# Kernel optimization log

Measured on AMD Instinct MI355X. Metric: run time of the kernel, lower is better.

Reference implementation:

```python
import jax, jax.numpy as jnp
import numpy as np

IN_C = 64
OUT_C = 64
NUM_RELS = 32
N_NODES = 20000
N_EDGES = 50000


def setup_inputs() -> dict:
    key = jax.random.key(0)
    k1, k2, k3, k4, k5, k6, k7 = jax.random.split(key, 7)
    x = jax.random.normal(k1, (N_NODES, IN_C), dtype=jnp.float32)
    edge_index = jax.random.randint(k2, (2, N_EDGES), 0, N_NODES, dtype=jnp.int64)
    edge_type = jax.random.randint(k3, (N_EDGES,), 0, NUM_RELS, dtype=jnp.int64)
    weight_fwd = jax.random.normal(k4, (NUM_RELS, IN_C * OUT_C), dtype=jnp.float32)
    weight_bwd = jax.random.normal(k5, (NUM_RELS, IN_C * OUT_C), dtype=jnp.float32)
    lin_w = jax.random.normal(k6, (OUT_C, IN_C), dtype=jnp.float32) * (1.0 / np.sqrt(IN_C))
    lin_b = jax.random.normal(k7, (OUT_C,), dtype=jnp.float32) * 0.01
    return {"x": x, "edge_index": edge_index, "edge_type": edge_type,
            "weight_fwd": weight_fwd, "weight_bwd": weight_bwd,
            "lin_w": lin_w, "lin_b": lin_b}


def type_gcn_conv(x, src, dst, edge_type, weight_table):
    # degrees[e] = (# edges sharing src[e]) + 1  (faithful to pairwise-compare count)
    n_nodes = x.shape[0]
    counts = jax.ops.segment_sum(jnp.ones(src.shape[0], jnp.float32), src,
                                 num_segments=n_nodes)
    degrees = counts[src] + 1.0                      # [E]
    w = weight_table[edge_type]                      # [E, in*out] gather
    w = w / (jnp.linalg.norm(w, axis=1, keepdims=True) + 0.01)
    w = w / degrees[:, None]
    w = w.reshape(-1, IN_C, OUT_C)                   # [E, in, out]
    msg = jnp.einsum('ei,eio->eo', x[src], w)        # per-edge small matmul
    return jax.ops.segment_sum(msg, dst, num_segments=n_nodes)  # scatter-add at dst


def reference(x, edge_index, edge_type, weight_fwd, weight_bwd, lin_w, lin_b):
    src, dst = edge_index[0], edge_index[1]
    fwd = type_gcn_conv(x, src, dst, edge_type, weight_fwd)
    # backward conv sees reversed edge_index: its src is original dst
    bwd = type_gcn_conv(x, dst, src, edge_type, weight_bwd)
    return x @ lin_w.T + lin_b + fwd + bwd
```

## Files before the change

### kernel.cpp

```cpp
#include <hip/hip_runtime.h>

#define NREL 32

typedef short short8 __attribute__((ext_vector_type(8)));
typedef float f32x4 __attribute__((ext_vector_type(4)));

__device__ inline unsigned short f2bf(float f) {
    union { float f; unsigned u; } u; u.f = f;
    unsigned r = u.u + 0x7FFF + ((u.u >> 16) & 1);
    return (unsigned short)(r >> 16);
}

__device__ inline void bucket_scan(const int* __restrict__ hist, int lane,
                                   int& h, int& P, int& excl) {
    h = (lane < NREL) ? hist[lane] : 0;
    P = ((h + 63) >> 6) << 6;
    int s = P;
    #pragma unroll
    for (int off = 1; off < 32; off <<= 1) {
        int t = __shfl_up(s, off, 64);
        if ((lane & 31) >= off) s += t;
    }
    excl = s - P;
}


__global__ __launch_bounds__(256) void setup_kernel(
        const float* __restrict__ x,
        const int* __restrict__ src, const int* __restrict__ dst,
        const int* __restrict__ et,
        const float* __restrict__ wf, const float* __restrict__ wb,
        const float* __restrict__ lw, const float* __restrict__ lb,
        float* __restrict__ cntf, float* __restrict__ cntb,
        int* __restrict__ hist, unsigned short* __restrict__ wtb,
        unsigned short* __restrict__ xbf,
        float* __restrict__ out, int E, int N, int nCountB) {
    __shared__ float smem[4 * 8 * 64 + 8];
    int tid = threadIdx.x;
    int b = blockIdx.x;

    if (b < nCountB) {
        int* lh = (int*)smem;
        if (tid < NREL) lh[tid] = 0;
        __syncthreads();
        int e = b * 256 + tid;
        if (e < E) {
            atomicAdd(&cntf[src[e]], 1.0f);
            atomicAdd(&cntb[dst[e]], 1.0f);
            atomicAdd(&lh[et[e]], 1);
        }
        __syncthreads();
        if (tid < NREL && lh[tid]) atomicAdd(&hist[tid], lh[tid]);
        return;
    }
    b -= nCountB;
    if (b < 64) {
        int rel = b & 31, tab = b >> 5;
        const float* s_ = (tab ? wb : wf) + rel * 4096;
        unsigned short* d_ = wtb + (size_t)b * 4096;
        float* part = smem;
        float ssum = 0.f;
        #pragma unroll
        for (int k = 0; k < 16; k += 4) {
            float4 v = *(const float4*)(s_ + tid * 16 + k);
            ssum += v.x * v.x + v.y * v.y + v.z * v.z + v.w * v.w;
        }
        #pragma unroll
        for (int off = 32; off >= 1; off >>= 1) ssum += __shfl_down(ssum, off, 64);
        if ((tid & 63) == 0) part[tid >> 6] = ssum;
        __syncthreads();
        if (tid == 0) part[4] = 1.0f / (sqrtf(part[0] + part[1] + part[2] + part[3]) + 0.01f);
        __syncthreads();
        float sc = part[4];
        int i = tid >> 2, o0 = (tid & 3) * 16;
        #pragma unroll
        for (int q = 0; q < 4; ++q) {
            float4 v = *(const float4*)(s_ + i * 64 + o0 + q * 4);
            d_[(o0 + q * 4 + 0) * 64 + i] = f2bf(v.x * sc);
            d_[(o0 + q * 4 + 1) * 64 + i] = f2bf(v.y * sc);
            d_[(o0 + q * 4 + 2) * 64 + i] = f2bf(v.z * sc);
            d_[(o0 + q * 4 + 3) * 64 + i] = f2bf(v.w * sc);
        }
        return;
    }
    b -= 64;
    {
        int lane = tid & 63, w = tid >> 6;
        int nodeBase = b * 32 + w * 8;
        float4 wrow[16];
        const float4* lwrow = (const float4*)(lw + lane * 64);
        #pragma unroll
        for (int g = 0; g < 16; ++g) wrow[g] = lwrow[g];
        float bias = lb[lane];
        float* xs = smem + w * 8 * 64;
        #pragma unroll
        for (int t = 0; t < 8; ++t) {
            int n = nodeBase + t;
            if (n < N) {
                float v = x[(size_t)n * 64 + lane];
                xs[t * 64 + lane] = v;
                xbf[(size_t)n * 64 + lane] = f2bf(v);
            }
        }
        __syncthreads();
        for (int t = 0; t < 8; ++t) {
            int n = nodeBase + t;
            if (n >= N) break;
            float acc = bias;
            const float4* xr = (const float4*)(xs + t * 64);
            #pragma unroll
            for (int g = 0; g < 16; ++g) {
                float4 xv = xr[g];
                acc = fmaf(xv.x, wrow[g].x, acc);
                acc = fmaf(xv.y, wrow[g].y, acc);
                acc = fmaf(xv.z, wrow[g].z, acc);
                acc = fmaf(xv.w, wrow[g].w, acc);
            }
            out[(size_t)n * 64 + lane] = acc;
        }
    }
}

__global__ void scatter_kernel(const int* __restrict__ src, const int* __restrict__ dst,
                               const int* __restrict__ et,
                               const float* __restrict__ cntf, const float* __restrict__ cntb,
                               int* __restrict__ fill, const int* __restrict__ hist,
                               int4* __restrict__ einfo, int E) {
    __shared__ int lh[NREL];
    __shared__ int lbase[NREL];
    __shared__ int bstartS[NREL];
    int tid = threadIdx.x;
    if (tid < 64) {
        int h, P, excl;
        bucket_scan(hist, tid, h, P, excl);
        if (tid < NREL) bstartS[tid] = excl;
    }
    if (tid < NREL) lh[tid] = 0;
    __syncthreads();
    int e = blockIdx.x * blockDim.x + tid;
    int r = 0, my = 0;
    bool valid = (e < E);
    if (valid) { r = et[e]; my = atomicAdd(&lh[r], 1); }
    __syncthreads();
    if (tid < NREL && lh[tid]) lbase[tid] = atomicAdd(&fill[tid], lh[tid]);
    __syncthreads();
    if (valid) {
        int s = src[e], d = dst[e];
        float invf = 1.0f / (cntf[s] + 1.0f);
        float invb = 1.0f / (cntb[d] + 1.0f);
        einfo[bstartS[r] + lbase[r] + my] =
            make_int4(s, d, __float_as_int(invf), __float_as_int(invb));
    }
}

#define APITCH 72
__global__ __launch_bounds__(256) void conv_mfma(
        const unsigned short* __restrict__ xbf,
        const int* __restrict__ hist,
        const unsigned short* __restrict__ wtb,
        const int4* __restrict__ einfo,
        float* __restrict__ out) {
    int tid = threadIdx.x;
    int lane = tid & 63;
    int h, P, excl;
    bucket_scan(hist, lane, h, P, excl);
    int pos = blockIdx.x * 64;
    unsigned long long m_ = __ballot(lane < NREL && pos >= excl && pos < excl + P);
    if (m_ == 0) return;
    int rel = __ffsll(m_) - 1;
    int start = __shfl(excl, rel, 64);
    int hr = __shfl(h, rel, 64);
    int valid = hr - (pos - start);
    if (valid > 64) valid = 64;
    int dir = blockIdx.y;

    __shared__ unsigned short As[64 * APITCH];
    __shared__ unsigned short Bs[64 * APITCH];
    __shared__ int dstS[64];
    __shared__ float invS[64];

    int j = tid >> 2, part = tid & 3;

    {
        const uint4* s4 = (const uint4*)(wtb + (size_t)((dir << 5) + rel) * 4096 + j * 64 + part * 16);
        uint4 v0 = s4[0], v1 = s4[1];
        *(uint4*)(&Bs[j * APITCH + part * 16]) = v0;
        *(uint4*)(&Bs[j * APITCH + part * 16 + 8]) = v1;
    }

    if (j >= valid) {
        uint4 z = {0, 0, 0, 0};
        *(uint4*)(&As[j * APITCH + part * 16]) = z;
        *(uint4*)(&As[j * APITCH + part * 16 + 8]) = z;
        if (part == 0) { dstS[j] = -1; invS[j] = 0.f; }
    } else {
        int4 v = einfo[pos + j];
        int s_ = dir ? v.y : v.x;
        int d_ = dir ? v.x : v.y;
        float inv = __int_as_float(dir ? v.w : v.z);
        const uint4* xr = (const uint4*)(xbf + (size_t)s_ * 64);
        uint4 a0 = xr[part * 2], a1 = xr[part * 2 + 1];
        *(uint4*)(&As[j * APITCH + part * 16]) = a0;
        *(uint4*)(&As[j * APITCH + part * 16 + 8]) = a1;
        if (part == 0) { dstS[j] = d_; invS[j] = inv; }
    }
    __syncthreads();

    int w = tid >> 6;
    int m = lane & 15, quad = lane >> 4;
    f32x4 acc0 = {0.f, 0.f, 0.f, 0.f}, acc1 = acc0, acc2 = acc0, acc3 = acc0;
    #pragma unroll
    for (int k0 = 0; k0 < 64; k0 += 32) {
        short8 a  = *(const short8*)(&As[(w * 16 + m) * APITCH + k0 + quad * 8]);
        short8 b0 = *(const short8*)(&Bs[(0  + m) * APITCH + k0 + quad * 8]);
        short8 b1 = *(const short8*)(&Bs[(16 + m) * APITCH + k0 + quad * 8]);
        short8 b2 = *(const short8*)(&Bs[(32 + m) * APITCH + k0 + quad * 8]);
        short8 b3 = *(const short8*)(&Bs[(48 + m) * APITCH + k0 + quad * 8]);
        acc0 = __builtin_amdgcn_mfma_f32_16x16x32_bf16(a, b0, acc0, 0, 0, 0);
        acc1 = __builtin_amdgcn_mfma_f32_16x16x32_bf16(a, b1, acc1, 0, 0, 0);
        acc2 = __builtin_amdgcn_mfma_f32_16x16x32_bf16(a, b2, acc2, 0, 0, 0);
        acc3 = __builtin_amdgcn_mfma_f32_16x16x32_bf16(a, b3, acc3, 0, 0, 0);
    }

    int row_base = w * 16 + quad * 4;
    #pragma unroll
    for (int r = 0; r < 4; ++r) {
        int row = row_base + r;
        int d_ = dstS[row];
        if (d_ >= 0) {
            float inv = invS[row];
            float* op = out + (size_t)d_ * 64 + m;
            atomicAdd(op +  0, acc0[r] * inv);
            atomicAdd(op + 16, acc1[r] * inv);
            atomicAdd(op + 32, acc2[r] * inv);
            atomicAdd(op + 48, acc3[r] * inv);
        }
    }
}

extern "C" void kernel_launch(void* const* d_in, const int* in_sizes, int n_in,
                              void* d_out, int out_size, void* d_ws, size_t ws_size,
                              hipStream_t stream) {
    const float* x  = (const float*)d_in[0];
    const int*   ei = (const int*)  d_in[1];
    const int*   et = (const int*)  d_in[2];
    const float* wf = (const float*)d_in[3];
    const float* wb = (const float*)d_in[4];
    const float* lw = (const float*)d_in[5];
    const float* lb = (const float*)d_in[6];
    float* out = (float*)d_out;

    const int E = in_sizes[2];
    const int N = in_sizes[0] / 64;
    const int maxC = ((E + 63) >> 6) + NREL;

    char* p = (char*)d_ws;
    unsigned short* wtb = (unsigned short*)p;  p += (size_t)2 * NREL * 4096 * sizeof(unsigned short);
    unsigned short* xbf = (unsigned short*)p;  p += (size_t)N * 64 * sizeof(unsigned short);
    float* cntf = (float*)p;                   p += (size_t)N * sizeof(float);
    float* cntb = (float*)p;                   p += (size_t)N * sizeof(float);
    int*   hist = (int*)p;                     p += NREL * sizeof(int);
    int*   fill = (int*)p;                     p += NREL * sizeof(int);
    int4*  einfo = (int4*)p;                   p += (size_t)maxC * 64 * sizeof(int4);

    const int* srcp = ei;
    const int* dstp = ei + E;

    hipMemsetAsync(cntf, 0, ((size_t)2 * N + 2 * NREL) * sizeof(float), stream);

    const int nCountB = (E + 255) / 256;
    const int nLinB   = (N + 31) / 32;
    setup_kernel<<<nCountB + 64 + nLinB, 256, 0, stream>>>(
        x, srcp, dstp, et, wf, wb, lw, lb, cntf, cntb, hist, wtb, xbf, out, E, N, nCountB);
    scatter_kernel<<<(E + 255) / 256, 256, 0, stream>>>(
        srcp, dstp, et, cntf, cntb, fill, hist, einfo, E);
    dim3 cgrid(maxC, 2);
    conv_mfma<<<cgrid, 256, 0, stream>>>(xbf, hist, wtb, einfo, out);
}
```

Before: 115.0 us.

## Fuse setup, scatter and conv into one persistent kernel with grid barriers

Replaces the memset and the three kernel launches with a single persistent kernel of 768 blocks. Software grid barriers built on global atomics separate the zeroing, counting/weight-prep/linear, bucket-scatter and MFMA conv phases, which removes launch gaps between them. The conv phase now loads A and B operands straight from global memory into MFMA registers instead of staging them through LDS. The design assumes all 768 blocks are co-resident (launch bounds of 3 blocks per CU). If they are not, the barriers deadlock, and the spin-waits add synchronisation overhead.

```diff
diff --git a/kernel.cpp b/kernel.cpp
--- a/kernel.cpp
+++ b/kernel.cpp
@@ -24,216 +24,216 @@
     excl = s - P;
 }
 
-
-__global__ __launch_bounds__(256) void setup_kernel(
+__device__ inline void grid_barrier(int* bar, int target) {
+    __syncthreads();
+    if (threadIdx.x == 0) {
+        __hip_atomic_fetch_add(bar, 1, __ATOMIC_RELEASE, __HIP_MEMORY_SCOPE_AGENT);
+        while (__hip_atomic_load(bar, __ATOMIC_ACQUIRE, __HIP_MEMORY_SCOPE_AGENT) < target)
+            __builtin_amdgcn_s_sleep(2);
+    }
+    __syncthreads();
+}
+
+
+__global__ __launch_bounds__(256, 3) void fused_kernel(
         const float* __restrict__ x,
         const int* __restrict__ src, const int* __restrict__ dst,
         const int* __restrict__ et,
         const float* __restrict__ wf, const float* __restrict__ wb,
         const float* __restrict__ lw, const float* __restrict__ lb,
-        float* __restrict__ cntf, float* __restrict__ cntb,
-        int* __restrict__ hist, unsigned short* __restrict__ wtb,
-        unsigned short* __restrict__ xbf,
-        float* __restrict__ out, int E, int N, int nCountB) {
+        unsigned short* wtb, unsigned short* xbf,
+        float* cntf, float* cntb, int* hist, int* fill,
+        int* bar, int4* einfo, float* out,
+        int E, int N, int nCountB, int nLinB) {
     __shared__ float smem[4 * 8 * 64 + 8];
     int tid = threadIdx.x;
-    int b = blockIdx.x;
-
-    if (b < nCountB) {
+    int lane = tid & 63;
+    const int G = gridDim.x;
+
+    {
+        int tot = 2 * N + 2 * NREL;
+        for (int i = blockIdx.x * 256 + tid; i < tot; i += G * 256) cntf[i] = 0.f;
+    }
+    grid_barrier(bar, G);
+
+    int totalRoles = nCountB + 64 + nLinB;
+    for (int b = blockIdx.x; b < totalRoles; b += G) {
+        if (b < nCountB) {
+            int* lh = (int*)smem;
+            if (tid < NREL) lh[tid] = 0;
+            __syncthreads();
+            int e = b * 256 + tid;
+            if (e < E) {
+                atomicAdd(&cntf[src[e]], 1.0f);
+                atomicAdd(&cntb[dst[e]], 1.0f);
+                atomicAdd(&lh[et[e]], 1);
+            }
+            __syncthreads();
+            if (tid < NREL && lh[tid]) atomicAdd(&hist[tid], lh[tid]);
+        } else if (b < nCountB + 64) {
+            int b2 = b - nCountB;
+            int rel = b2 & 31, tab = b2 >> 5;
+            const float* s_ = (tab ? wb : wf) + rel * 4096;
+            unsigned short* d_ = wtb + (size_t)b2 * 4096;
+            float* part = smem;
+            float ssum = 0.f;
+            #pragma unroll
+            for (int k = 0; k < 16; k += 4) {
+                float4 v = *(const float4*)(s_ + tid * 16 + k);
+                ssum += v.x * v.x + v.y * v.y + v.z * v.z + v.w * v.w;
+            }
+            #pragma unroll
+            for (int off = 32; off >= 1; off >>= 1) ssum += __shfl_down(ssum, off, 64);
+            if ((tid & 63) == 0) part[tid >> 6] = ssum;
+            __syncthreads();
+            if (tid == 0) part[4] = 1.0f / (sqrtf(part[0] + part[1] + part[2] + part[3]) + 0.01f);
+            __syncthreads();
+            float sc = part[4];
+            int i = tid >> 2, o0 = (tid & 3) * 16;
+            #pragma unroll
+            for (int q = 0; q < 4; ++q) {
+                float4 v = *(const float4*)(s_ + i * 64 + o0 + q * 4);
+                d_[(o0 + q * 4 + 0) * 64 + i] = f2bf(v.x * sc);
+                d_[(o0 + q * 4 + 1) * 64 + i] = f2bf(v.y * sc);
+                d_[(o0 + q * 4 + 2) * 64 + i] = f2bf(v.z * sc);
+                d_[(o0 + q * 4 + 3) * 64 + i] = f2bf(v.w * sc);
+            }
+        } else {
+            int b3 = b - nCountB - 64;
+            int w = tid >> 6;
+            int nodeBase = b3 * 32 + w * 8;
+            float4 wrow[16];
+            const float4* lwrow = (const float4*)(lw + lane * 64);
+            #pragma unroll
+            for (int g = 0; g < 16; ++g) wrow[g] = lwrow[g];
+            float bias = lb[lane];
+            float* xs = smem + w * 8 * 64;
+            #pragma unroll
+            for (int t = 0; t < 8; ++t) {
+                int n = nodeBase + t;
+                if (n < N) {
+                    float v = x[(size_t)n * 64 + lane];
+                    xs[t * 64 + lane] = v;
+                    xbf[(size_t)n * 64 + lane] = f2bf(v);
+                }
+            }
+            __syncthreads();
+            for (int t = 0; t < 8; ++t) {
+                int n = nodeBase + t;
+                if (n >= N) break;
+                float acc = bias;
+                const float4* xr = (const float4*)(xs + t * 64);
+                #pragma unroll
+                for (int g = 0; g < 16; ++g) {
+                    float4 xv = xr[g];
+                    acc = fmaf(xv.x, wrow[g].x, acc);
+                    acc = fmaf(xv.y, wrow[g].y, acc);
+                    acc = fmaf(xv.z, wrow[g].z, acc);
+                    acc = fmaf(xv.w, wrow[g].w, acc);
+                }
+                out[(size_t)n * 64 + lane] = acc;
+            }
+        }
+        __syncthreads();
+    }
+    grid_barrier(bar, 2 * G);
+
+    {
         int* lh = (int*)smem;
-        if (tid < NREL) lh[tid] = 0;
+        int* lbase = lh + NREL;
+        int* bstartS = lh + 2 * NREL;
+        if (tid < 64) {
+            int h2, P2, excl2;
+            bucket_scan(hist, tid, h2, P2, excl2);
+            if (tid < NREL) bstartS[tid] = excl2;
+        }
         __syncthreads();
-        int e = b * 256 + tid;
-        if (e < E) {
-            atomicAdd(&cntf[src[e]], 1.0f);
-            atomicAdd(&cntb[dst[e]], 1.0f);
-            atomicAdd(&lh[et[e]], 1);
-        }
-        __syncthreads();
-        if (tid < NREL && lh[tid]) atomicAdd(&hist[tid], lh[tid]);
-        return;
-    }
-    b -= nCountB;
-    if (b < 64) {
-        int rel = b & 31, tab = b >> 5;
-        const float* s_ = (tab ? wb : wf) + rel * 4096;
-        unsigned short* d_ = wtb + (size_t)b * 4096;
-        float* part = smem;
-        float ssum = 0.f;
-        #pragma unroll
-        for (int k = 0; k < 16; k += 4) {
-            float4 v = *(const float4*)(s_ + tid * 16 + k);
-            ssum += v.x * v.x + v.y * v.y + v.z * v.z + v.w * v.w;
-        }
-        #pragma unroll
-        for (int off = 32; off >= 1; off >>= 1) ssum += __shfl_down(ssum, off, 64);
-        if ((tid & 63) == 0) part[tid >> 6] = ssum;
-        __syncthreads();
-        if (tid == 0) part[4] = 1.0f / (sqrtf(part[0] + part[1] + part[2] + part[3]) + 0.01f);
-        __syncthreads();
-        float sc = part[4];
-        int i = tid >> 2, o0 = (tid & 3) * 16;
-        #pragma unroll
-        for (int q = 0; q < 4; ++q) {
-            float4 v = *(const float4*)(s_ + i * 64 + o0 + q * 4);
-            d_[(o0 + q * 4 + 0) * 64 + i] = f2bf(v.x * sc);
-            d_[(o0 + q * 4 + 1) * 64 + i] = f2bf(v.y * sc);
-            d_[(o0 + q * 4 + 2) * 64 + i] = f2bf(v.z * sc);
-            d_[(o0 + q * 4 + 3) * 64 + i] = f2bf(v.w * sc);
-        }
-        return;
-    }
-    b -= 64;
+        for (int b = blockIdx.x; b < nCountB; b += G) {
+            if (tid < NREL) lh[tid] = 0;
+            __syncthreads();
+            int e = b * 256 + tid;
+            int r = 0, my = 0;
+            bool valid = (e < E);
+            if (valid) { r = et[e]; my = atomicAdd(&lh[r], 1); }
+            __syncthreads();
+            if (tid < NREL && lh[tid]) lbase[tid] = atomicAdd(&fill[tid], lh[tid]);
+            __syncthreads();
+            if (valid) {
+                int s = src[e], d = dst[e];
+                float invf = 1.0f / (cntf[s] + 1.0f);
+                float invb = 1.0f / (cntb[d] + 1.0f);
+                einfo[bstartS[r] + lbase[r] + my] =
+                    make_int4(s, d, __float_as_int(invf), __float_as_int(invb));
+            }
+            __syncthreads();
+        }
+    }
+    grid_barrier(bar, 3 * G);
+
     {
-        int lane = tid & 63, w = tid >> 6;
-        int nodeBase = b * 32 + w * 8;
-        float4 wrow[16];
-        const float4* lwrow = (const float4*)(lw + lane * 64);
-        #pragma unroll
-        for (int g = 0; g < 16; ++g) wrow[g] = lwrow[g];
-        float bias = lb[lane];
-        float* xs = smem + w * 8 * 64;
-        #pragma unroll
-        for (int t = 0; t < 8; ++t) {
-            int n = nodeBase + t;
-            if (n < N) {
-                float v = x[(size_t)n * 64 + lane];
-                xs[t * 64 + lane] = v;
-                xbf[(size_t)n * 64 + lane] = f2bf(v);
-            }
-        }
-        __syncthreads();
-        for (int t = 0; t < 8; ++t) {
-            int n = nodeBase + t;
-            if (n >= N) break;
-            float acc = bias;
-            const float4* xr = (const float4*)(xs + t * 64);
-            #pragma unroll
-            for (int g = 0; g < 16; ++g) {
-                float4 xv = xr[g];
-                acc = fmaf(xv.x, wrow[g].x, acc);
-                acc = fmaf(xv.y, wrow[g].y, acc);
-                acc = fmaf(xv.z, wrow[g].z, acc);
-                acc = fmaf(xv.w, wrow[g].w, acc);
-            }
-            out[(size_t)n * 64 + lane] = acc;
-        }
-    }
-}
-
-__global__ void scatter_kernel(const int* __restrict__ src, const int* __restrict__ dst,
-                               const int* __restrict__ et,
-                               const float* __restrict__ cntf, const float* __restrict__ cntb,
-                               int* __restrict__ fill, const int* __restrict__ hist,
-                               int4* __restrict__ einfo, int E) {
-    __shared__ int lh[NREL];
-    __shared__ int lbase[NREL];
-    __shared__ int bstartS[NREL];
-    int tid = threadIdx.x;
-    if (tid < 64) {
         int h, P, excl;
-        bucket_scan(hist, tid, h, P, excl);
-        if (tid < NREL) bstartS[tid] = excl;
-    }
-    if (tid < NREL) lh[tid] = 0;
-    __syncthreads();
-    int e = blockIdx.x * blockDim.x + tid;
-    int r = 0, my = 0;
-    bool valid = (e < E);
-    if (valid) { r = et[e]; my = atomicAdd(&lh[r], 1); }
-    __syncthreads();
-    if (tid < NREL && lh[tid]) lbase[tid] = atomicAdd(&fill[tid], lh[tid]);
-    __syncthreads();
-    if (valid) {
-        int s = src[e], d = dst[e];
-        float invf = 1.0f / (cntf[s] + 1.0f);
-        float invb = 1.0f / (cntb[d] + 1.0f);
-        einfo[bstartS[r] + lbase[r] + my] =
-            make_int4(s, d, __float_as_int(invf), __float_as_int(invb));
-    }
-}
-
-#define APITCH 72
-__global__ __launch_bounds__(256) void conv_mfma(
-        const unsigned short* __restrict__ xbf,
-        const int* __restrict__ hist,
-        const unsigned short* __restrict__ wtb,
-        const int4* __restrict__ einfo,
-        float* __restrict__ out) {
-    int tid = threadIdx.x;
-    int lane = tid & 63;
-    int h, P, excl;
-    bucket_scan(hist, lane, h, P, excl);
-    int pos = blockIdx.x * 64;
-    unsigned long long m_ = __ballot(lane < NREL && pos >= excl && pos < excl + P);
-    if (m_ == 0) return;
-    int rel = __ffsll(m_) - 1;
-    int start = __shfl(excl, rel, 64);
-    int hr = __shfl(h, rel, 64);
-    int valid = hr - (pos - start);
-    if (valid > 64) valid = 64;
-    int dir = blockIdx.y;
-
-    __shared__ unsigned short As[64 * APITCH];
-    __shared__ unsigned short Bs[64 * APITCH];
-    __shared__ int dstS[64];
-    __shared__ float invS[64];
-
-    int j = tid >> 2, part = tid & 3;
-
-    {
-        const uint4* s4 = (const uint4*)(wtb + (size_t)((dir << 5) + rel) * 4096 + j * 64 + part * 16);
-        uint4 v0 = s4[0], v1 = s4[1];
-        *(uint4*)(&Bs[j * APITCH + part * 16]) = v0;
-        *(uint4*)(&Bs[j * APITCH + part * 16 + 8]) = v1;
-    }
-
-    if (j >= valid) {
-        uint4 z = {0, 0, 0, 0};
-        *(uint4*)(&As[j * APITCH + part * 16]) = z;
-        *(uint4*)(&As[j * APITCH + part * 16 + 8]) = z;
-        if (part == 0) { dstS[j] = -1; invS[j] = 0.f; }
-    } else {
-        int4 v = einfo[pos + j];
-        int s_ = dir ? v.y : v.x;
-        int d_ = dir ? v.x : v.y;
-        float inv = __int_as_float(dir ? v.w : v.z);
-        const uint4* xr = (const uint4*)(xbf + (size_t)s_ * 64);
-        uint4 a0 = xr[part * 2], a1 = xr[part * 2 + 1];
-        *(uint4*)(&As[j * APITCH + part * 16]) = a0;
-        *(uint4*)(&As[j * APITCH + part * 16 + 8]) = a1;
-        if (part == 0) { dstS[j] = d_; invS[j] = inv; }
-    }
-    __syncthreads();
-
-    int w = tid >> 6;
-    int m = lane & 15, quad = lane >> 4;
-    f32x4 acc0 = {0.f, 0.f, 0.f, 0.f}, acc1 = acc0, acc2 = acc0, acc3 = acc0;
-    #pragma unroll
-    for (int k0 = 0; k0 < 64; k0 += 32) {
-        short8 a  = *(const short8*)(&As[(w * 16 + m) * APITCH + k0 + quad * 8]);
-        short8 b0 = *(const short8*)(&Bs[(0  + m) * APITCH + k0 + quad * 8]);
-        short8 b1 = *(const short8*)(&Bs[(16 + m) * APITCH + k0 + quad * 8]);
-        short8 b2 = *(const short8*)(&Bs[(32 + m) * APITCH + k0 + quad * 8]);
-        short8 b3 = *(const short8*)(&Bs[(48 + m) * APITCH + k0 + quad * 8]);
-        acc0 = __builtin_amdgcn_mfma_f32_16x16x32_bf16(a, b0, acc0, 0, 0, 0);
-        acc1 = __builtin_amdgcn_mfma_f32_16x16x32_bf16(a, b1, acc1, 0, 0, 0);
-        acc2 = __builtin_amdgcn_mfma_f32_16x16x32_bf16(a, b2, acc2, 0, 0, 0);
-        acc3 = __builtin_amdgcn_mfma_f32_16x16x32_bf16(a, b3, acc3, 0, 0, 0);
-    }
-
-    int row_base = w * 16 + quad * 4;
-    #pragma unroll
-    for (int r = 0; r < 4; ++r) {
-        int row = row_base + r;
-        int d_ = dstS[row];
-        if (d_ >= 0) {
-            float inv = invS[row];
-            float* op = out + (size_t)d_ * 64 + m;
-            atomicAdd(op +  0, acc0[r] * inv);
-            atomicAdd(op + 16, acc1[r] * inv);
-            atomicAdd(op + 32, acc2[r] * inv);
-            atomicAdd(op + 48, acc3[r] * inv);
+        bucket_scan(hist, lane, h, P, excl);
+        int totChunks = __shfl(excl + P, 31, 64) >> 6;
+        int w = tid >> 6, m = lane & 15, quad = (lane >> 4) & 3;
+
+        for (int c = blockIdx.x; c < 2 * totChunks; c += G) {
+            int dir = (c >= totChunks);
+            int cid = dir ? c - totChunks : c;
+            int pos = cid * 64;
+            unsigned long long mm = __ballot(lane < NREL && pos >= excl && pos < excl + P);
+            int rel = __ffsll(mm) - 1;
+            int start = __shfl(excl, rel, 64);
+            int hr = __shfl(h, rel, 64);
+            int valid = hr - (pos - start);
+            if (valid > 64) valid = 64;
+
+            int row = w * 16 + m;
+            int4 v = einfo[pos + (row < valid ? row : 0)];
+            int s_ = dir ? v.y : v.x;
+            int d_ = dir ? v.x : v.y;
+            float inv = __int_as_float(dir ? v.w : v.z);
+
+            const unsigned short* xr = xbf + (size_t)s_ * 64 + quad * 8;
+            short8 a0 = *(const short8*)(xr);
+            short8 a1 = *(const short8*)(xr + 32);
+
+            const unsigned short* bb = wtb + (size_t)((dir << 5) + rel) * 4096
+                                           + m * 64 + quad * 8;
+            f32x4 acc0 = {0.f, 0.f, 0.f, 0.f}, acc1 = acc0, acc2 = acc0, acc3 = acc0;
+            {
+                short8 b0 = *(const short8*)(bb);
+                short8 b1 = *(const short8*)(bb + 1024);
+                short8 b2 = *(const short8*)(bb + 2048);
+                short8 b3 = *(const short8*)(bb + 3072);
+                acc0 = __builtin_amdgcn_mfma_f32_16x16x32_bf16(a0, b0, acc0, 0, 0, 0);
+                acc1 = __builtin_amdgcn_mfma_f32_16x16x32_bf16(a0, b1, acc1, 0, 0, 0);
+                acc2 = __builtin_amdgcn_mfma_f32_16x16x32_bf16(a0, b2, acc2, 0, 0, 0);
+                acc3 = __builtin_amdgcn_mfma_f32_16x16x32_bf16(a0, b3, acc3, 0, 0, 0);
+            }
+            {
+                short8 b0 = *(const short8*)(bb + 32);
+                short8 b1 = *(const short8*)(bb + 1024 + 32);
+                short8 b2 = *(const short8*)(bb + 2048 + 32);
+                short8 b3 = *(const short8*)(bb + 3072 + 32);
+                acc0 = __builtin_amdgcn_mfma_f32_16x16x32_bf16(a1, b0, acc0, 0, 0, 0);
+                acc1 = __builtin_amdgcn_mfma_f32_16x16x32_bf16(a1, b1, acc1, 0, 0, 0);
+                acc2 = __builtin_amdgcn_mfma_f32_16x16x32_bf16(a1, b2, acc2, 0, 0, 0);
+                acc3 = __builtin_amdgcn_mfma_f32_16x16x32_bf16(a1, b3, acc3, 0, 0, 0);
+            }
+
+            #pragma unroll
+            for (int r = 0; r < 4; ++r) {
+                int qq = quad * 4 + r;
+                int dd = __shfl(d_, qq, 64);
+                float iv = __shfl(inv, qq, 64);
+                if (w * 16 + qq < valid) {
+                    float* op = out + (size_t)dd * 64 + m;
+                    atomicAdd(op +  0, acc0[r] * iv);
+                    atomicAdd(op + 16, acc1[r] * iv);
+                    atomicAdd(op + 32, acc2[r] * iv);
+                    atomicAdd(op + 48, acc3[r] * iv);
+                }
+            }
         }
     }
 }
@@ -261,19 +261,18 @@
     float* cntb = (float*)p;                   p += (size_t)N * sizeof(float);
     int*   hist = (int*)p;                     p += NREL * sizeof(int);
     int*   fill = (int*)p;                     p += NREL * sizeof(int);
+    int*   bar  = (int*)p;                     p += 4 * sizeof(int);
     int4*  einfo = (int4*)p;                   p += (size_t)maxC * 64 * sizeof(int4);
 
     const int* srcp = ei;
     const int* dstp = ei + E;
 
-    hipMemsetAsync(cntf, 0, ((size_t)2 * N + 2 * NREL) * sizeof(float), stream);
+    hipMemsetAsync(bar, 0, sizeof(int), stream);
 
     const int nCountB = (E + 255) / 256;
     const int nLinB   = (N + 31) / 32;
-    setup_kernel<<<nCountB + 64 + nLinB, 256, 0, stream>>>(
-        x, srcp, dstp, et, wf, wb, lw, lb, cntf, cntb, hist, wtb, xbf, out, E, N, nCountB);
-    scatter_kernel<<<(E + 255) / 256, 256, 0, stream>>>(
-        srcp, dstp, et, cntf, cntb, fill, hist, einfo, E);
-    dim3 cgrid(maxC, 2);
-    conv_mfma<<<cgrid, 256, 0, stream>>>(xbf, hist, wtb, einfo, out);
-}
+    fused_kernel<<<768, 256, 0, stream>>>(
+        x, srcp, dstp, et, wf, wb, lw, lb,
+        wtb, xbf, cntf, cntb, hist, fill, bar, einfo, out,
+        E, N, nCountB, nLinB);
+}
```

Result: slower. 319.5 us (+177.9%).

## Fuse edge bucketing into setup kernel with fixed-capacity per-relation buckets

Applied to the files above, without the earlier changes.

Drops the separate scatter kernel. The counting blocks in the setup kernel now write (src,dst) pairs directly into fixed-capacity per-relation buckets, replacing the histogram-then-prefix-scan placement. The conv kernel derives chunk offsets from the fill counts and computes the inverse degree itself by reading cntf/cntb. This removes one launch and one pass over the edges, and shrinks edge records from int4 to int2. In exchange the workspace grows to NREL*CAP entries and the conv kernel does extra dependent count loads, which must see completed counts since it runs after the setup kernel.

```diff
diff --git a/kernel.cpp b/kernel.cpp
--- a/kernel.cpp
+++ b/kernel.cpp
@@ -9,19 +9,6 @@
     union { float f; unsigned u; } u; u.f = f;
     unsigned r = u.u + 0x7FFF + ((u.u >> 16) & 1);
     return (unsigned short)(r >> 16);
-}
-
-__device__ inline void bucket_scan(const int* __restrict__ hist, int lane,
-                                   int& h, int& P, int& excl) {
-    h = (lane < NREL) ? hist[lane] : 0;
-    P = ((h + 63) >> 6) << 6;
-    int s = P;
-    #pragma unroll
-    for (int off = 1; off < 32; off <<= 1) {
-        int t = __shfl_up(s, off, 64);
-        if ((lane & 31) >= off) s += t;
-    }
-    excl = s - P;
 }
 
 
@@ -32,25 +19,31 @@
         const float* __restrict__ wf, const float* __restrict__ wb,
         const float* __restrict__ lw, const float* __restrict__ lb,
         float* __restrict__ cntf, float* __restrict__ cntb,
-        int* __restrict__ hist, unsigned short* __restrict__ wtb,
-        unsigned short* __restrict__ xbf,
-        float* __restrict__ out, int E, int N, int nCountB) {
+        int* __restrict__ fill, unsigned short* __restrict__ wtb,
+        unsigned short* __restrict__ xbf, int2* __restrict__ einfo,
+        float* __restrict__ out, int E, int N, int nCountB, int CAP) {
     __shared__ float smem[4 * 8 * 64 + 8];
     int tid = threadIdx.x;
     int b = blockIdx.x;
 
     if (b < nCountB) {
         int* lh = (int*)smem;
-        if (tid < NREL) lh[tid] = 0;
+        int* lbase = lh + NREL;
+        if (tid < 2 * NREL) lh[tid] = 0;
         __syncthreads();
         int e = b * 256 + tid;
-        if (e < E) {
-            atomicAdd(&cntf[src[e]], 1.0f);
-            atomicAdd(&cntb[dst[e]], 1.0f);
-            atomicAdd(&lh[et[e]], 1);
-        }
-        __syncthreads();
-        if (tid < NREL && lh[tid]) atomicAdd(&hist[tid], lh[tid]);
+        int s = 0, d = 0, r = 0, my = 0;
+        bool valid = (e < E);
+        if (valid) {
+            s = src[e]; d = dst[e]; r = et[e];
+            atomicAdd(&cntf[s], 1.0f);
+            atomicAdd(&cntb[d], 1.0f);
+            my = atomicAdd(&lh[r], 1);
+        }
+        __syncthreads();
+        if (tid < NREL && lh[tid]) lbase[tid] = atomicAdd(&fill[tid], lh[tid]);
+        __syncthreads();
+        if (valid) einfo[r * CAP + lbase[r] + my] = make_int2(s, d);
         return;
     }
     b -= nCountB;
@@ -121,56 +114,35 @@
     }
 }
 
-__global__ void scatter_kernel(const int* __restrict__ src, const int* __restrict__ dst,
-                               const int* __restrict__ et,
-                               const float* __restrict__ cntf, const float* __restrict__ cntb,
-                               int* __restrict__ fill, const int* __restrict__ hist,
-                               int4* __restrict__ einfo, int E) {
-    __shared__ int lh[NREL];
-    __shared__ int lbase[NREL];
-    __shared__ int bstartS[NREL];
-    int tid = threadIdx.x;
-    if (tid < 64) {
-        int h, P, excl;
-        bucket_scan(hist, tid, h, P, excl);
-        if (tid < NREL) bstartS[tid] = excl;
-    }
-    if (tid < NREL) lh[tid] = 0;
-    __syncthreads();
-    int e = blockIdx.x * blockDim.x + tid;
-    int r = 0, my = 0;
-    bool valid = (e < E);
-    if (valid) { r = et[e]; my = atomicAdd(&lh[r], 1); }
-    __syncthreads();
-    if (tid < NREL && lh[tid]) lbase[tid] = atomicAdd(&fill[tid], lh[tid]);
-    __syncthreads();
-    if (valid) {
-        int s = src[e], d = dst[e];
-        float invf = 1.0f / (cntf[s] + 1.0f);
-        float invb = 1.0f / (cntb[d] + 1.0f);
-        einfo[bstartS[r] + lbase[r] + my] =
-            make_int4(s, d, __float_as_int(invf), __float_as_int(invb));
-    }
-}
-
 #define APITCH 72
 __global__ __launch_bounds__(256) void conv_mfma(
         const unsigned short* __restrict__ xbf,
-        const int* __restrict__ hist,
+        const float* __restrict__ cntf, const float* __restrict__ cntb,
+        const int* __restrict__ fill,
         const unsigned short* __restrict__ wtb,
-        const int4* __restrict__ einfo,
-        float* __restrict__ out) {
+        const int2* __restrict__ einfo,
+        float* __restrict__ out, int CAP) {
     int tid = threadIdx.x;
     int lane = tid & 63;
-    int h, P, excl;
-    bucket_scan(hist, lane, h, P, excl);
-    int pos = blockIdx.x * 64;
-    unsigned long long m_ = __ballot(lane < NREL && pos >= excl && pos < excl + P);
-    if (m_ == 0) return;
-    int rel = __ffsll(m_) - 1;
-    int start = __shfl(excl, rel, 64);
-    int hr = __shfl(h, rel, 64);
-    int valid = hr - (pos - start);
+
+    int fr = (lane < NREL) ? fill[lane] : 0;
+    int ch = (fr + 63) >> 6;
+    int s_scan = ch;
+    #pragma unroll
+    for (int off = 1; off < 32; off <<= 1) {
+        int t = __shfl_up(s_scan, off, 64);
+        if ((lane & 31) >= off) s_scan += t;
+    }
+    int chExcl = s_scan - ch;
+
+    int c = blockIdx.x;
+    unsigned long long mm = __ballot(lane < NREL && c >= chExcl && c < chExcl + ch);
+    if (mm == 0) return;
+    int rel = __ffsll(mm) - 1;
+    int lc = c - __shfl(chExcl, rel, 64);
+    int frr = __shfl(fr, rel, 64);
+    int pos = rel * CAP + lc * 64;
+    int valid = frr - lc * 64;
     if (valid > 64) valid = 64;
     int dir = blockIdx.y;
 
@@ -194,15 +166,18 @@
         *(uint4*)(&As[j * APITCH + part * 16 + 8]) = z;
         if (part == 0) { dstS[j] = -1; invS[j] = 0.f; }
     } else {
-        int4 v = einfo[pos + j];
+        int2 v = einfo[pos + j];
         int s_ = dir ? v.y : v.x;
         int d_ = dir ? v.x : v.y;
-        float inv = __int_as_float(dir ? v.w : v.z);
         const uint4* xr = (const uint4*)(xbf + (size_t)s_ * 64);
         uint4 a0 = xr[part * 2], a1 = xr[part * 2 + 1];
         *(uint4*)(&As[j * APITCH + part * 16]) = a0;
         *(uint4*)(&As[j * APITCH + part * 16 + 8]) = a1;
-        if (part == 0) { dstS[j] = d_; invS[j] = inv; }
+        if (part == 0) {
+            float cv = dir ? cntb[s_] : cntf[s_];
+            dstS[j] = d_;
+            invS[j] = 1.0f / (cv + 1.0f);
+        }
     }
     __syncthreads();
 
@@ -252,6 +227,7 @@
 
     const int E = in_sizes[2];
     const int N = in_sizes[0] / 64;
+    const int CAP = ((E + 63) >> 6) << 6;
     const int maxC = ((E + 63) >> 6) + NREL;
 
     char* p = (char*)d_ws;
@@ -259,21 +235,19 @@
     unsigned short* xbf = (unsigned short*)p;  p += (size_t)N * 64 * sizeof(unsigned short);
     float* cntf = (float*)p;                   p += (size_t)N * sizeof(float);
     float* cntb = (float*)p;                   p += (size_t)N * sizeof(float);
-    int*   hist = (int*)p;                     p += NREL * sizeof(int);
     int*   fill = (int*)p;                     p += NREL * sizeof(int);
-    int4*  einfo = (int4*)p;                   p += (size_t)maxC * 64 * sizeof(int4);
+    int2*  einfo = (int2*)p;                   p += (size_t)NREL * CAP * sizeof(int2);
 
     const int* srcp = ei;
     const int* dstp = ei + E;
 
-    hipMemsetAsync(cntf, 0, ((size_t)2 * N + 2 * NREL) * sizeof(float), stream);
+    hipMemsetAsync(cntf, 0, ((size_t)2 * N + NREL) * sizeof(float), stream);
 
     const int nCountB = (E + 255) / 256;
     const int nLinB   = (N + 31) / 32;
     setup_kernel<<<nCountB + 64 + nLinB, 256, 0, stream>>>(
-        x, srcp, dstp, et, wf, wb, lw, lb, cntf, cntb, hist, wtb, xbf, out, E, N, nCountB);
-    scatter_kernel<<<(E + 255) / 256, 256, 0, stream>>>(
-        srcp, dstp, et, cntf, cntb, fill, hist, einfo, E);
+        x, srcp, dstp, et, wf, wb, lw, lb, cntf, cntb, fill, wtb, xbf, einfo,
+        out, E, N, nCountB, CAP);
     dim3 cgrid(maxC, 2);
-    conv_mfma<<<cgrid, 256, 0, stream>>>(xbf, hist, wtb, einfo, out);
-}
+    conv_mfma<<<cgrid, 256, 0, stream>>>(xbf, cntf, cntb, fill, wtb, einfo, out, CAP);
+}
```

After: 112.2 us. -2.4%, faster.
